# Performance work log

Hardware: AMD Instinct MI355X
Metric: run time of the kernel (lower is better)

Reference implementation:

```python
import jax, jax.numpy as jnp
import numpy as np

S, B, C = 7, 2, 4
N = 5 * B + C
LAMBDA_BOX = LAMBDA_CLS = LAMBDA_DF = 1.0
BATCH = 16384


def setup_inputs() -> dict:
    key = jax.random.key(0)
    k1, k2, k3 = jax.random.split(key, 3)
    shape = (BATCH, S, S, N)
    pred = jax.random.uniform(k1, shape, jnp.float32, 0.02, 0.98)
    target = jax.random.uniform(k2, shape, jnp.float32, 0.02, 0.98)
    obj = (jax.random.uniform(k3, (BATCH, S, S)) < 0.3).astype(jnp.float32)
    # confidence channels of both target bboxes carry the 0/1 object indicator
    target = target.at[..., 4].set(obj).at[..., 9].set(obj)
    return {"pred_tensor": pred, "target_tensor": target}


def _bce(p, t):
    # elementwise binary cross entropy (sum applied by caller)
    return -(t * jnp.log(p) + (1.0 - t) * jnp.log(1.0 - p))


def reference(pred_tensor, target_tensor):
    conf_t = target_tensor[..., 4]                       # [b,S,S]
    coord = (conf_t > 0).astype(pred_tensor.dtype)       # object cells

    pb = pred_tensor[..., :5 * B].reshape(*pred_tensor.shape[:-1], B, 5)   # [b,S,S,B,5]
    tb = target_tensor[..., :5 * B].reshape(*target_tensor.shape[:-1], B, 5)

    # xywh (cell coords) -> xyxy (image coords), as in the torch loop
    p_xy = pb[..., :2] / S
    p_wh = pb[..., 2:4]
    p_lt = p_xy - 0.5 * p_wh
    p_rb = p_xy + 0.5 * p_wh
    t0 = tb[..., 0, :]                                   # first target box of the group
    t_xy = t0[..., :2] / S
    t_wh = t0[..., 2:4]
    t_lt = t_xy - 0.5 * t_wh
    t_rb = t_xy + 0.5 * t_wh

    lt = jnp.maximum(p_lt, t_lt[..., None, :])
    rb = jnp.minimum(p_rb, t_rb[..., None, :])
    wh = jnp.clip(rb - lt, 0.0)
    inter = wh[..., 0] * wh[..., 1]                      # [b,S,S,B]
    area_p = (p_rb[..., 0] - p_lt[..., 0]) * (p_rb[..., 1] - p_lt[..., 1])
    area_t = ((t_rb[..., 0] - t_lt[..., 0]) * (t_rb[..., 1] - t_lt[..., 1]))[..., None]
    iou = inter / (area_p + area_t - inter)              # [b,S,S,B]

    max_iou = jnp.max(iou, axis=-1)                      # [b,S,S]
    idx = jnp.argmax(iou, axis=-1)                       # responsible bbox index
    resp_p = jnp.take_along_axis(pb, idx[..., None, None], axis=-2)[..., 0, :]  # [b,S,S,5]
    resp_t = jnp.take_along_axis(tb, idx[..., None, None], axis=-2)[..., 0, :]

    loss_xy = jnp.sum(coord * jnp.sum((resp_p[..., :2] - resp_t[..., :2]) ** 2, -1))
    loss_wh = jnp.sum(coord * jnp.sum((jnp.sqrt(resp_p[..., 2:4]) - jnp.sqrt(resp_t[..., 2:4])) ** 2, -1))
    loss_obj = jnp.sum(coord * (resp_p[..., 4] - max_iou) ** 2)

    loss_cls = jnp.sum(coord[..., None] * _bce(pred_tensor[..., 5 * B:], target_tensor[..., 5 * B:]))

    # focal-style df term over ALL cells (the original triple loop)
    q = conf_t
    p = pred_tensor[..., 4]
    alpha = (1.0 - q) / (1.0 - p)
    loss_df = jnp.sum(alpha * (p - q) * jnp.log(p) + (q - p) * jnp.log(1.0 - p))

    total = LAMBDA_BOX * (loss_xy + loss_wh + loss_obj) + LAMBDA_CLS * loss_cls + LAMBDA_DF * loss_df
    return total
```

## Files before the change

kernel.cpp:

```cpp
#include <hip/hip_runtime.h>


#define NPAIRS (16384 * 7 * 7 / 2)
#define TPB 64
#define PPB 64
#define SLOTS (PPB * 7)
#define NBLOCKS (NPAIRS / PPB)

typedef __attribute__((address_space(3))) void lds_void;
typedef const __attribute__((address_space(1))) void glb_void;

__device__ __forceinline__ float cell_loss(const float* __restrict__ p,
                                           const float* __restrict__ t) {
    const float conf_t = t[4];
    const float coord = (conf_t > 0.0f) ? 1.0f : 0.0f;

    const float tx = t[0] / 7.0f;
    const float ty = t[1] / 7.0f;
    const float tw = t[2];
    const float th = t[3];
    const float tlx = tx - 0.5f * tw, tly = ty - 0.5f * th;
    const float trx = tx + 0.5f * tw, trY = ty + 0.5f * th;
    const float area_t = (trx - tlx) * (trY - tly);

    float iou0, iou1;
    {
        const float px = p[0] / 7.0f, py = p[1] / 7.0f;
        const float pw = p[2], ph = p[3];
        const float plx = px - 0.5f * pw, ply = py - 0.5f * ph;
        const float prx = px + 0.5f * pw, prY = py + 0.5f * ph;
        const float ltx = fmaxf(plx, tlx), lty = fmaxf(ply, tly);
        const float rbx = fminf(prx, trx), rby = fminf(prY, trY);
        const float wx = fmaxf(rbx - ltx, 0.0f), wy = fmaxf(rby - lty, 0.0f);
        const float inter = wx * wy;
        const float area_p = (prx - plx) * (prY - ply);
        iou0 = inter / (area_p + area_t - inter);
    }
    {
        const float px = p[5] / 7.0f, py = p[6] / 7.0f;
        const float pw = p[7], ph = p[8];
        const float plx = px - 0.5f * pw, ply = py - 0.5f * ph;
        const float prx = px + 0.5f * pw, prY = py + 0.5f * ph;
        const float ltx = fmaxf(plx, tlx), lty = fmaxf(ply, tly);
        const float rbx = fminf(prx, trx), rby = fminf(prY, trY);
        const float wx = fmaxf(rbx - ltx, 0.0f), wy = fmaxf(rby - lty, 0.0f);
        const float inter = wx * wy;
        const float area_p = (prx - plx) * (prY - ply);
        iou1 = inter / (area_p + area_t - inter);
    }

    const bool sel1 = (iou1 > iou0);
    const float max_iou = fmaxf(iou0, iou1);

    const float rp0 = sel1 ? p[5] : p[0];
    const float rp1 = sel1 ? p[6] : p[1];
    const float rp2 = sel1 ? p[7] : p[2];
    const float rp3 = sel1 ? p[8] : p[3];
    const float rp4 = sel1 ? p[9] : p[4];
    const float rt0 = sel1 ? t[5] : t[0];
    const float rt1 = sel1 ? t[6] : t[1];
    const float rt2 = sel1 ? t[7] : t[2];
    const float rt3 = sel1 ? t[8] : t[3];

    const float dx = rp0 - rt0;
    const float dy = rp1 - rt1;
    const float l_xy = dx * dx + dy * dy;

    const float sw = sqrtf(rp2) - sqrtf(rt2);
    const float sh = sqrtf(rp3) - sqrtf(rt3);
    const float l_wh = sw * sw + sh * sh;

    const float dobj = rp4 - max_iou;
    const float l_obj = dobj * dobj;

    float l_cls = 0.0f;
#pragma unroll
    for (int c = 10; c < 14; ++c) {
        const float pc = p[c];
        const float tc = t[c];
        l_cls += -(tc * logf(pc) + (1.0f - tc) * logf(1.0f - pc));
    }

    const float q = conf_t;
    const float pp = p[4];
    const float alpha = (1.0f - q) / (1.0f - pp);
    const float l_df = alpha * (pp - q) * logf(pp) + (q - pp) * logf(1.0f - pp);

    return coord * (l_xy + l_wh + l_obj + l_cls) + l_df;
}

__global__ __launch_bounds__(TPB) void yolo_loss_kernel(
    const float* __restrict__ pred, const float* __restrict__ tgt,
    float* __restrict__ partials) {
    __shared__ float4 sp[SLOTS];
    __shared__ float4 st[SLOTS];

    const int lane = threadIdx.x;

    const long base4 = (long)blockIdx.x * SLOTS;
    const float4* __restrict__ gp = reinterpret_cast<const float4*>(pred) + base4;
    const float4* __restrict__ gt = reinterpret_cast<const float4*>(tgt) + base4;

#pragma unroll
    for (int it = 0; it < 7; ++it) {
        const int s = it * 64;
        __builtin_amdgcn_global_load_lds((glb_void*)(gp + s + lane),
                                         (lds_void*)(sp + s), 16, 0, 0);
        __builtin_amdgcn_global_load_lds((glb_void*)(gt + s + lane),
                                         (lds_void*)(st + s), 16, 0, 0);
    }
    asm volatile("s_waitcnt vmcnt(0)" ::: "memory");

    float lp[28];
    float lt[28];
#pragma unroll
    for (int j = 0; j < 7; ++j) {
        const int s = 7 * lane + j;
        reinterpret_cast<float4*>(lp)[j] = sp[s];
        reinterpret_cast<float4*>(lt)[j] = st[s];
    }

    float v = cell_loss(lp, lt) + cell_loss(lp + 14, lt + 14);

#pragma unroll
    for (int off = 32; off > 0; off >>= 1) v += __shfl_down(v, off, 64);
    if (lane == 0) partials[blockIdx.x] = v;
}

__global__ __launch_bounds__(256) void reduce_kernel(
    const float* __restrict__ partials, float* __restrict__ out) {
    const int tid = threadIdx.x;
    float v = 0.0f;
    for (int i = tid; i < NBLOCKS; i += 256) v += partials[i];
#pragma unroll
    for (int off = 32; off > 0; off >>= 1) v += __shfl_down(v, off, 64);
    __shared__ float s[4];
    const int lane = tid & 63;
    const int wid = tid >> 6;
    if (lane == 0) s[wid] = v;
    __syncthreads();
    if (tid == 0) out[0] = s[0] + s[1] + s[2] + s[3];
}

extern "C" void kernel_launch(void* const* d_in, const int* in_sizes, int n_in,
                              void* d_out, int out_size, void* d_ws, size_t ws_size,
                              hipStream_t stream) {
    const float* pred = (const float*)d_in[0];
    const float* tgt  = (const float*)d_in[1];
    float* out = (float*)d_out;
    float* partials = (float*)d_ws;

    yolo_loss_kernel<<<NBLOCKS, TPB, 0, stream>>>(pred, tgt, partials);
    reduce_kernel<<<1, 256, 0, stream>>>(partials, out);
}
```

Baseline: 110.2 us.

## Process two chunks per block with split waitcnt and widen final reduction

```diff
diff --git a/kernel.cpp b/kernel.cpp
--- a/kernel.cpp
+++ b/kernel.cpp
@@ -3,8 +3,9 @@
 
 #define NPAIRS (16384 * 7 * 7 / 2)
 #define TPB 64
-#define PPB 64
-#define SLOTS (PPB * 7)
+#define PPW 64
+#define PPB (2 * PPW)
+#define SLOTS (PPW * 7)
 #define NBLOCKS (NPAIRS / PPB)
 
 typedef __attribute__((address_space(3))) void lds_void;
@@ -92,54 +93,78 @@
 __global__ __launch_bounds__(TPB) void yolo_loss_kernel(
     const float* __restrict__ pred, const float* __restrict__ tgt,
     float* __restrict__ partials) {
-    __shared__ float4 sp[SLOTS];
-    __shared__ float4 st[SLOTS];
+    __shared__ float4 sp[2][SLOTS];
+    __shared__ float4 st[2][SLOTS];
 
     const int lane = threadIdx.x;
 
-    const long base4 = (long)blockIdx.x * SLOTS;
+    const long base4 = (long)blockIdx.x * (2 * SLOTS);
     const float4* __restrict__ gp = reinterpret_cast<const float4*>(pred) + base4;
     const float4* __restrict__ gt = reinterpret_cast<const float4*>(tgt) + base4;
 
 #pragma unroll
-    for (int it = 0; it < 7; ++it) {
-        const int s = it * 64;
-        __builtin_amdgcn_global_load_lds((glb_void*)(gp + s + lane),
-                                         (lds_void*)(sp + s), 16, 0, 0);
-        __builtin_amdgcn_global_load_lds((glb_void*)(gt + s + lane),
-                                         (lds_void*)(st + s), 16, 0, 0);
-    }
-    asm volatile("s_waitcnt vmcnt(0)" ::: "memory");
-
-    float lp[28];
-    float lt[28];
+    for (int h = 0; h < 2; ++h) {
 #pragma unroll
-    for (int j = 0; j < 7; ++j) {
-        const int s = 7 * lane + j;
-        reinterpret_cast<float4*>(lp)[j] = sp[s];
-        reinterpret_cast<float4*>(lt)[j] = st[s];
+        for (int it = 0; it < 7; ++it) {
+            const int s = h * SLOTS + it * 64;
+            const int d = it * 64;
+            __builtin_amdgcn_global_load_lds((glb_void*)(gp + s + lane),
+                                             (lds_void*)(&sp[h][d]), 16, 0, 0);
+            __builtin_amdgcn_global_load_lds((glb_void*)(gt + s + lane),
+                                             (lds_void*)(&st[h][d]), 16, 0, 0);
+        }
     }
 
-    float v = cell_loss(lp, lt) + cell_loss(lp + 14, lt + 14);
+    float v = 0.0f;
+
+    asm volatile("s_waitcnt vmcnt(14)" ::: "memory");
+    {
+        float lp[28], lt[28];
+#pragma unroll
+        for (int j = 0; j < 7; ++j) {
+            const int s = 7 * lane + j;
+            reinterpret_cast<float4*>(lp)[j] = sp[0][s];
+            reinterpret_cast<float4*>(lt)[j] = st[0][s];
+        }
+        v += cell_loss(lp, lt) + cell_loss(lp + 14, lt + 14);
+    }
+
+    asm volatile("s_waitcnt vmcnt(0)" ::: "memory");
+    {
+        float lp[28], lt[28];
+#pragma unroll
+        for (int j = 0; j < 7; ++j) {
+            const int s = 7 * lane + j;
+            reinterpret_cast<float4*>(lp)[j] = sp[1][s];
+            reinterpret_cast<float4*>(lt)[j] = st[1][s];
+        }
+        v += cell_loss(lp, lt) + cell_loss(lp + 14, lt + 14);
+    }
 
 #pragma unroll
     for (int off = 32; off > 0; off >>= 1) v += __shfl_down(v, off, 64);
     if (lane == 0) partials[blockIdx.x] = v;
 }
 
-__global__ __launch_bounds__(256) void reduce_kernel(
-    const float* __restrict__ partials, float* __restrict__ out) {
+__global__ __launch_bounds__(1024) void reduce_kernel(
+    const float4* __restrict__ partials4, float* __restrict__ out) {
     const int tid = threadIdx.x;
     float v = 0.0f;
-    for (int i = tid; i < NBLOCKS; i += 256) v += partials[i];
+    if (tid < NBLOCKS / 4) {
+        const float4 x = partials4[tid];
+        v = (x.x + x.y) + (x.z + x.w);
+    }
 #pragma unroll
     for (int off = 32; off > 0; off >>= 1) v += __shfl_down(v, off, 64);
-    __shared__ float s[4];
-    const int lane = tid & 63;
-    const int wid = tid >> 6;
-    if (lane == 0) s[wid] = v;
+    __shared__ float s[16];
+    if ((tid & 63) == 0) s[tid >> 6] = v;
     __syncthreads();
-    if (tid == 0) out[0] = s[0] + s[1] + s[2] + s[3];
+    if (tid == 0) {
+        float r = 0.0f;
+#pragma unroll
+        for (int i = 0; i < 16; ++i) r += s[i];
+        out[0] = r;
+    }
 }
 
 extern "C" void kernel_launch(void* const* d_in, const int* in_sizes, int n_in,
@@ -151,5 +176,6 @@
     float* partials = (float*)d_ws;
 
     yolo_loss_kernel<<<NBLOCKS, TPB, 0, stream>>>(pred, tgt, partials);
-    reduce_kernel<<<1, 256, 0, stream>>>(partials, out);
+    reduce_kernel<<<1, 1024, 0, stream>>>(
+        reinterpret_cast<const float4*>(partials), out);
 }
```

After: 110.3 us. No clear change (+0.2%).
